# Optimization experiments

Measured on AMD Instinct MI355X. Metric: run time of the kernel, lower is better.

The kernel has to match this reference:

```python
import jax, jax.numpy as jnp
import numpy as np

N_NODES = 100000
N_EDGES = 1600000
N_GRAPHS = 1024
IN_G, HID_G = 64, 128
IN_T, H1, H2 = 200, 256, 128
CONCAT = 2 * HID_G + H2  # 384


def setup_inputs() -> dict:
    key = jax.random.key(0)
    ks = jax.random.split(key, 24)
    def lin(k, fin, fout):
        kw, kb = jax.random.split(k)
        s = 1.0 / np.sqrt(fin)
        return (jax.random.uniform(kw, (fin, fout), jnp.float32, -s, s),
                jax.random.uniform(kb, (fout,), jnp.float32, -s, s))
    Wg1, bg1 = lin(ks[0], IN_G, HID_G)
    Wg2, bg2 = lin(ks[1], HID_G, HID_G)
    Wg3, bg3 = lin(ks[2], HID_G, HID_G)
    Wg4, bg4 = lin(ks[3], HID_G, HID_G)
    Wt1, bt1 = lin(ks[4], IN_T, H1)
    Wt2, bt2 = lin(ks[5], H1, H2)
    Wf1, bf1 = lin(ks[6], CONCAT, H1)
    Wf2, bf2 = lin(ks[7], H1, H2)
    Wf3, bf3 = lin(ks[8], H2, 1)
    x_graph = jax.random.normal(ks[9], (N_NODES, IN_G), jnp.float32)
    edge_index = jax.random.randint(ks[10], (2, N_EDGES), 0, N_NODES, jnp.int32)
    batch = jnp.sort(jax.random.randint(ks[11], (N_NODES,), 0, N_GRAPHS, jnp.int32))
    x_tabular = jax.random.normal(ks[12], (N_GRAPHS, IN_T), jnp.float32)
    return {"x_graph": x_graph, "edge_index": edge_index, "batch": batch,
            "x_tabular": x_tabular,
            "Wg1": Wg1, "bg1": bg1, "Wg2": Wg2, "bg2": bg2,
            "Wg3": Wg3, "bg3": bg3, "Wg4": Wg4, "bg4": bg4,
            "Wt1": Wt1, "bt1": bt1, "Wt2": Wt2, "bt2": bt2,
            "Wf1": Wf1, "bf1": bf1, "Wf2": Wf2, "bf2": bf2,
            "Wf3": Wf3, "bf3": bf3}


def _gcn(x, src, dst, norm, W, b, n):
    # x' = D^-1/2 A_hat D^-1/2 (x W) + b, scatter-add over edges
    h = x @ W
    msg = h[src] * norm[:, None]
    return jax.ops.segment_sum(msg, dst, num_segments=n) + b


def reference(x_graph, edge_index, batch, x_tabular,
              Wg1, bg1, Wg2, bg2, Wg3, bg3, Wg4, bg4,
              Wt1, bt1, Wt2, bt2, Wf1, bf1, Wf2, bf2, Wf3, bf3):
    n = x_graph.shape[0]
    b = x_tabular.shape[0]
    ar = jnp.arange(n, dtype=edge_index.dtype)
    # self-loops added once in Multi_Modal.forward + once inside GCNConv (default)
    src = jnp.concatenate([edge_index[0], ar, ar])
    dst = jnp.concatenate([edge_index[1], ar, ar])
    deg = jax.ops.segment_sum(jnp.ones(src.shape, x_graph.dtype), dst, num_segments=n)
    dinv = jnp.where(deg > 0, jax.lax.rsqrt(deg), 0.0)
    norm = dinv[src] * dinv[dst]
    h = jax.nn.relu(_gcn(x_graph, src, dst, norm, Wg1, bg1, n))
    h = jax.nn.relu(_gcn(h, src, dst, norm, Wg2, bg2, n))
    h = jax.nn.relu(_gcn(h, src, dst, norm, Wg3, bg3, n))
    h = jax.nn.relu(_gcn(h, src, dst, norm, Wg4, bg4, n))
    # global mean/max pool per graph
    cnt = jax.ops.segment_sum(jnp.ones((n,), h.dtype), batch, num_segments=b)
    mean = jax.ops.segment_sum(h, batch, num_segments=b) / jnp.maximum(cnt, 1.0)[:, None]
    mx = jax.ops.segment_max(h, batch, num_segments=b)
    x1 = jnp.concatenate([mean, mx], axis=1)
    # tabular branch
    x2 = jax.nn.relu(jax.nn.relu(x_tabular @ Wt1 + bt1) @ Wt2 + bt2)
    # fused head
    x = jnp.concatenate([x1, x2], axis=1)
    x = jax.nn.relu(x @ Wf1 + bf1)
    x = jax.nn.relu(x @ Wf2 + bf2)
    return jax.nn.sigmoid(x @ Wf3 + bf3)
```

## Files before the change

### kernel.cpp

```cpp
#include <hip/hip_runtime.h>
#include <hip/hip_bf16.h>
#include <math.h>

#define N_NODES  100000
#define N_EDGES  1600000
#define N_GRAPHS 1024

typedef __hip_bfloat16 bf16;
typedef unsigned short u16;
typedef unsigned int   u32;
typedef __attribute__((ext_vector_type(8))) short bf8_t;
typedef __attribute__((ext_vector_type(4))) float f4_t;

__device__ __forceinline__ float b2f(bf16 v) { return __bfloat162float(v); }
__device__ __forceinline__ u16 bfbits(float f) {
    bf16 h = __float2bfloat16(f);
    return *reinterpret_cast<u16*>(&h);
}
__device__ __forceinline__ float lo_bf(u32 u) { return __uint_as_float(u << 16); }
__device__ __forceinline__ float hi_bf(u32 u) { return __uint_as_float(u & 0xffff0000u); }

__global__ void sniff_dtype(const u16* __restrict__ p, int* __restrict__ flag) {
    if (blockIdx.x == 0 && threadIdx.x == 0) {
        int bad = 0;
        for (int i = 0; i < 256; ++i) {
            float f = __uint_as_float(((u32)p[i]) << 16);
            if (!(fabsf(f) < 100.f)) bad++;
        }
        *flag = (bad == 0) ? 1 : 0;
    }
}

#define NT 18
struct WTask { const void* src; void* dst; int n; int mode; int K; };
struct PrepArgs { WTask t[NT]; int bstart[NT]; };

__global__ void prep_k(PrepArgs args, const int* __restrict__ flag) {
    int b = blockIdx.x, ti = 0;
    while (ti < NT - 1 && b >= args.bstart[ti + 1]) ++ti;
    int idx = (b - args.bstart[ti]) * 256 + threadIdx.x;
    WTask tk = args.t[ti];
    if (idx >= tk.n) return;
    int isb = *flag;
    if (tk.mode == 0) {
        float v = isb ? b2f(((const bf16*)tk.src)[idx]) : ((const float*)tk.src)[idx];
        ((float*)tk.dst)[idx] = v;
    } else {
        int bseg = idx >> 9, r = idx & 511;
        int L = r >> 3, j = r & 7;
        int kb = bseg >> 3, tt = bseg & 7;
        int k = kb * 32 + ((L >> 4) << 3) + j;
        int n = (tt << 4) + (L & 15);
        int so = k * 128 + n;
        float v = isb ? b2f(((const bf16*)tk.src)[so]) : ((const float*)tk.src)[so];
        ((u16*)tk.dst)[idx] = bfbits(v);
    }
}

__global__ void cvt_b(const void* __restrict__ src, u16* __restrict__ dst,
                      int n, const int* __restrict__ flag) {
    int i = blockIdx.x * blockDim.x + threadIdx.x;
    if (i >= n) return;
    if (*flag) dst[i] = ((const u16*)src)[i];
    else       dst[i] = bfbits(((const float*)src)[i]);
}

__global__ void deg_init(int* degi) {
    int i = blockIdx.x * blockDim.x + threadIdx.x;
    if (i < N_NODES) degi[i] = 2;
}

__global__ void deg_edges(const int* __restrict__ dst, int* __restrict__ degi) {
    int e = blockIdx.x * blockDim.x + threadIdx.x;
    if (e < N_EDGES) atomicAdd(&degi[dst[e]], 1);
}

__global__ void dinv_k(const int* __restrict__ degi, float* __restrict__ dinv) {
    int i = blockIdx.x * blockDim.x + threadIdx.x;
    if (i < N_NODES) dinv[i] = rsqrtf((float)degi[i]);
}

#define SCAN_B 256
__global__ void scan1(const int* __restrict__ degi, int* __restrict__ ex,
                      int* __restrict__ bsum) {
    __shared__ int s[SCAN_B];
    int i = blockIdx.x * SCAN_B + threadIdx.x;
    int v = (i < N_NODES) ? (degi[i] - 2) : 0;
    s[threadIdx.x] = v;
    __syncthreads();
    for (int off = 1; off < SCAN_B; off <<= 1) {
        int t = (threadIdx.x >= off) ? s[threadIdx.x - off] : 0;
        __syncthreads();
        if (threadIdx.x >= off) s[threadIdx.x] += t;
        __syncthreads();
    }
    if (i < N_NODES) ex[i] = s[threadIdx.x] - v;
    if (threadIdx.x == SCAN_B - 1) bsum[blockIdx.x] = s[SCAN_B - 1];
}

__global__ void scan2(int* __restrict__ bsum, int nb) {
    __shared__ int s[512];
    int i = threadIdx.x;
    int v = (i < nb) ? bsum[i] : 0;
    s[i] = v;
    __syncthreads();
    for (int off = 1; off < 512; off <<= 1) {
        int t = (i >= off) ? s[i - off] : 0;
        __syncthreads();
        if (i >= off) s[i] += t;
        __syncthreads();
    }
    if (i < nb) bsum[i] = s[i] - v;
}

__global__ void scan3(int* __restrict__ rowptr, const int* __restrict__ bsum,
                      int* __restrict__ cnt) {
    int i = blockIdx.x * SCAN_B + threadIdx.x;
    if (i >= N_NODES) return;
    rowptr[i] += bsum[blockIdx.x];
    cnt[i] = 0;
}

__global__ void fill_csr(const int* __restrict__ src, const int* __restrict__ dst,
                         const float* __restrict__ dinv, const int* __restrict__ rowptr,
                         int* __restrict__ cnt, int2* __restrict__ csrp) {
    int e = blockIdx.x * 256 + threadIdx.x;
    if (e >= N_EDGES) return;
    int s = src[e], d = dst[e];
    int pos = rowptr[d] + atomicAdd(&cnt[d], 1);
    csrp[pos] = make_int2(s, __float_as_int(dinv[s] * dinv[d]));
}

template<int K, bool EPI>
__global__ __launch_bounds__(256) void gemm_mfma(const u16* __restrict__ A,
        const u16* __restrict__ Wm, const float* __restrict__ bias,
        u16* __restrict__ Out, int M)
{
    int wave = threadIdx.x >> 6, lane = threadIdx.x & 63;
    int rowBase = blockIdx.x * 64 + wave * 16;
    int quad = lane >> 4, low = lane & 15;
    int arow = rowBase + low;
    if (arow >= M) arow = M - 1;
    const u16* ap = A + (size_t)arow * K + quad * 8;

    f4_t acc[8];
#pragma unroll
    for (int t = 0; t < 8; ++t) acc[t] = (f4_t)(0.f);

#pragma unroll
    for (int kb = 0; kb < K / 32; ++kb) {
        bf8_t a = *(const bf8_t*)(ap + kb * 32);
#pragma unroll
        for (int t = 0; t < 8; ++t) {
            bf8_t b = *(const bf8_t*)(Wm + (((kb << 3) + t) << 9) + lane * 8);
            acc[t] = __builtin_amdgcn_mfma_f32_16x16x32_bf16(a, b, acc[t], 0, 0, 0);
        }
    }

    int orow0 = rowBase + quad * 4;
#pragma unroll
    for (int t = 0; t < 8; ++t) {
        float bn = EPI ? bias[t * 16 + low] : 0.f;
#pragma unroll
        for (int j = 0; j < 4; ++j) {
            int r = orow0 + j;
            float v = acc[t][j];
            if (EPI) v = fmaxf(v + bn, 0.f);
            if (r < M) Out[(size_t)r * 128 + t * 16 + low] = bfbits(v);
        }
    }
}

__global__ __launch_bounds__(256) void gather_x(
        const int* __restrict__ rowptr, const int* __restrict__ cnt,
        const int2* __restrict__ csrp, const u16* __restrict__ X,
        const float* __restrict__ dinv, u16* __restrict__ G)
{
    int node = blockIdx.x * 4 + (threadIdx.x >> 6);
    if (node >= N_NODES) return;
    int lane = threadIdx.x & 63;
    int half = lane >> 5, fi = lane & 31;
    const u32* X2 = (const u32*)X;
    float accx = 0.f, accy = 0.f;
    if (half == 0) {
        float dv = dinv[node];
        float s = 2.f * dv * dv;
        u32 h0 = X2[(size_t)node * 32 + fi];
        accx = s * lo_bf(h0); accy = s * hi_bf(h0);
    }
    int rp = rowptr[node];
    int end = rp + cnt[node];
    int p = rp + half;
    for (; p + 8 <= end; p += 8) {
        int2 m0 = csrp[p],     m1 = csrp[p + 2];
        int2 m2 = csrp[p + 4], m3 = csrp[p + 6];
        u32 v0 = X2[(size_t)m0.x * 32 + fi];
        u32 v1 = X2[(size_t)m1.x * 32 + fi];
        u32 v2 = X2[(size_t)m2.x * 32 + fi];
        u32 v3 = X2[(size_t)m3.x * 32 + fi];
        float w0 = __int_as_float(m0.y), w1 = __int_as_float(m1.y);
        float w2 = __int_as_float(m2.y), w3 = __int_as_float(m3.y);
        accx += w0 * lo_bf(v0) + w1 * lo_bf(v1) + w2 * lo_bf(v2) + w3 * lo_bf(v3);
        accy += w0 * hi_bf(v0) + w1 * hi_bf(v1) + w2 * hi_bf(v2) + w3 * hi_bf(v3);
    }
    for (; p < end; p += 2) {
        int2 m = csrp[p];
        u32 v = X2[(size_t)m.x * 32 + fi];
        float w = __int_as_float(m.y);
        accx += w * lo_bf(v); accy += w * hi_bf(v);
    }
    accx += __shfl_xor(accx, 32);
    accy += __shfl_xor(accy, 32);
    if (half == 0) {
        u32 pack = ((u32)bfbits(accy) << 16) | (u32)bfbits(accx);
        ((u32*)G)[(size_t)node * 32 + fi] = pack;
    }
}

__global__ __launch_bounds__(256) void gather_agg(
        const int* __restrict__ rowptr, const int* __restrict__ cnt,
        const int2* __restrict__ csrp, const u16* __restrict__ H,
        const float* __restrict__ dinv, const float* __restrict__ bias,
        u16* __restrict__ A)
{
    int node = blockIdx.x * 4 + (threadIdx.x >> 6);
    if (node >= N_NODES) return;
    int lane = threadIdx.x & 63;
    const u32* H2 = (const u32*)H;
    float2 bb = ((const float2*)bias)[lane];
    float dv = dinv[node];
    float selfw = 2.f * dv * dv;
    u32 h0 = H2[(size_t)node * 64 + lane];
    float accx = bb.x + selfw * lo_bf(h0);
    float accy = bb.y + selfw * hi_bf(h0);
    int p = rowptr[node];
    int end = p + cnt[node];
    for (; p + 8 <= end; p += 8) {
        int2 m0 = csrp[p],     m1 = csrp[p + 1];
        int2 m2 = csrp[p + 2], m3 = csrp[p + 3];
        int2 m4 = csrp[p + 4], m5 = csrp[p + 5];
        int2 m6 = csrp[p + 6], m7 = csrp[p + 7];
        u32 v0 = H2[(size_t)m0.x * 64 + lane];
        u32 v1 = H2[(size_t)m1.x * 64 + lane];
        u32 v2 = H2[(size_t)m2.x * 64 + lane];
        u32 v3 = H2[(size_t)m3.x * 64 + lane];
        u32 v4 = H2[(size_t)m4.x * 64 + lane];
        u32 v5 = H2[(size_t)m5.x * 64 + lane];
        u32 v6 = H2[(size_t)m6.x * 64 + lane];
        u32 v7 = H2[(size_t)m7.x * 64 + lane];
        float w0 = __int_as_float(m0.y), w1 = __int_as_float(m1.y);
        float w2 = __int_as_float(m2.y), w3 = __int_as_float(m3.y);
        float w4 = __int_as_float(m4.y), w5 = __int_as_float(m5.y);
        float w6 = __int_as_float(m6.y), w7 = __int_as_float(m7.y);
        accx += w0 * lo_bf(v0) + w1 * lo_bf(v1) + w2 * lo_bf(v2) + w3 * lo_bf(v3)
              + w4 * lo_bf(v4) + w5 * lo_bf(v5) + w6 * lo_bf(v6) + w7 * lo_bf(v7);
        accy += w0 * hi_bf(v0) + w1 * hi_bf(v1) + w2 * hi_bf(v2) + w3 * hi_bf(v3)
              + w4 * hi_bf(v4) + w5 * hi_bf(v5) + w6 * hi_bf(v6) + w7 * hi_bf(v7);
    }
    for (; p < end; ++p) {
        int2 m = csrp[p];
        u32 v = H2[(size_t)m.x * 64 + lane];
        float w = __int_as_float(m.y);
        accx += w * lo_bf(v); accy += w * hi_bf(v);
    }
    accx = fmaxf(accx, 0.f);
    accy = fmaxf(accy, 0.f);
    u32 pack = ((u32)bfbits(accy) << 16) | (u32)bfbits(accx);
    ((u32*)A)[(size_t)node * 64 + lane] = pack;
}

__global__ __launch_bounds__(128) void pool_k(const u16* __restrict__ A,
        const int* __restrict__ batch, float* __restrict__ concat)
{
    __shared__ int sb[2];
    int g = blockIdx.x;
    if (threadIdx.x == 0) {
        int lo = 0, hi = N_NODES;
        while (lo < hi) { int m = (lo + hi) >> 1; if (batch[m] < g) lo = m + 1; else hi = m; }
        sb[0] = lo;
        hi = N_NODES;
        while (lo < hi) { int m = (lo + hi) >> 1; if (batch[m] < g + 1) lo = m + 1; else hi = m; }
        sb[1] = lo;
    }
    __syncthreads();
    int start = sb[0], end = sb[1];
    int t = threadIdx.x;
    float sum = 0.f, mx = -3.4e38f;
    for (int n = start; n < end; ++n) {
        float v = __uint_as_float(((u32)A[(size_t)n * 128 + t]) << 16);
        sum += v; mx = fmaxf(mx, v);
    }
    int cnt = end - start;
    float mean = sum / (float)(cnt > 0 ? cnt : 1);
    if (cnt == 0) mx = 0.f;
    concat[g * 384 + t] = mean;
    concat[g * 384 + 128 + t] = mx;
}

template<int KD, bool EXT>
__global__ void rowmm(const void* __restrict__ Xv, int ldx,
                      const float* __restrict__ W, const float* __restrict__ bias,
                      float* __restrict__ out, int ldo, const int* __restrict__ flagp)
{
    extern __shared__ float xs[];
    int g = blockIdx.x;
    int col = threadIdx.x;
    int N = blockDim.x;
    const int isb = EXT ? *flagp : 0;
    for (int k = col; k < KD; k += N) {
        size_t off = (size_t)g * ldx + k;
        xs[k] = EXT ? (isb ? b2f(((const bf16*)Xv)[off]) : ((const float*)Xv)[off])
                    : ((const float*)Xv)[off];
    }
    __syncthreads();
    float acc = bias[col];
    for (int k = 0; k < KD; ++k)
        acc += xs[k] * W[(size_t)k * N + col];
    out[(size_t)g * ldo + col] = fmaxf(acc, 0.f);
}

__global__ __launch_bounds__(256) void head3(const float* __restrict__ u2,
        const float* __restrict__ Wf3, const float* __restrict__ bf3,
        void* __restrict__ out, const int* __restrict__ flagp)
{
    int g = blockIdx.x * 4 + (threadIdx.x >> 6);
    int lane = threadIdx.x & 63;
    float2 v = ((const float2*)(u2 + (size_t)g * 128))[lane];
    float2 w = ((const float2*)Wf3)[lane];
    float acc = v.x * w.x + v.y * w.y;
    for (int off = 32; off > 0; off >>= 1) acc += __shfl_down(acc, off);
    if (lane == 0) {
        float z = acc + bf3[0];
        float sg = 1.f / (1.f + expf(-z));
        if (*flagp) ((bf16*)out)[g] = __float2bfloat16(sg);
        else        ((float*)out)[g] = sg;
    }
}

extern "C" void kernel_launch(void* const* d_in, const int* in_sizes, int n_in,
                              void* d_out, int out_size, void* d_ws, size_t ws_size,
                              hipStream_t stream) {
    const void* x_graph    = d_in[0];
    const int*  edge_index = (const int*)d_in[1];
    const int*  batch      = (const int*)d_in[2];
    const void* x_tab      = d_in[3];

    const int* src  = edge_index;
    const int* dstp = edge_index + N_EDGES;

    char* wsp = (char*)d_ws;
    int*  flag = (int*)wsp;                      wsp += 16;
    u16*  A16  = (u16*)wsp;                      wsp += (size_t)N_NODES * 128 * 2;
    u16*  B16  = (u16*)wsp;                      wsp += (size_t)N_NODES * 128 * 2;
    u16*  X16  = (u16*)wsp;                      wsp += (size_t)N_NODES * 64 * 2;
    u16*  G16  = (u16*)wsp;                      wsp += (size_t)N_NODES * 64 * 2;
    u16*  Wm[4];
    Wm[0] = (u16*)wsp;                           wsp += 64 * 128 * 2;
    Wm[1] = (u16*)wsp;                           wsp += 128 * 128 * 2;
    Wm[2] = (u16*)wsp;                           wsp += 128 * 128 * 2;
    Wm[3] = (u16*)wsp;                           wsp += 128 * 128 * 2;
    float* p = (float*)wsp;
    float* bg1f = p; p += 128;
    float* bg2f = p; p += 128;
    float* bg3f = p; p += 128;
    float* bg4f = p; p += 128;
    float* Wt1f = p; p += 200 * 256; float* bt1f = p; p += 256;
    float* Wt2f = p; p += 256 * 128; float* bt2f = p; p += 128;
    float* Wf1f = p; p += 384 * 256; float* bf1f = p; p += 256;
    float* Wf2f = p; p += 256 * 128; float* bf2f = p; p += 128;
    float* Wf3f = p; p += 128;       float* bf3f = p; p += 4;
    int*   degi   = (int*)p;            p += N_NODES;
    float* dinv   = p;                  p += N_NODES;
    int*   rowptr = (int*)p;            p += N_NODES;
    int*   cnt    = (int*)p;            p += N_NODES;
    int*   bsum   = (int*)p;            p += 512;
    int2*  csrp   = (int2*)p;           p += 2 * N_EDGES;
    float* concat = p;                  p += N_GRAPHS * 384;
    float* t1     = p;                  p += N_GRAPHS * 256;
    float* u1     = p;                  p += N_GRAPHS * 256;
    float* u2     = p;                  p += N_GRAPHS * 128;

    sniff_dtype<<<1, 64, 0, stream>>>((const u16*)x_graph, flag);

    PrepArgs pa;
    auto setT = [&](int i, const void* s, void* d, int n, int mode, int K) {
        pa.t[i].src = s; pa.t[i].dst = d; pa.t[i].n = n; pa.t[i].mode = mode; pa.t[i].K = K;
    };
    setT(0,  d_in[4],  Wm[0], 64 * 128, 1, 64);
    setT(1,  d_in[6],  Wm[1], 128 * 128, 1, 128);
    setT(2,  d_in[8],  Wm[2], 128 * 128, 1, 128);
    setT(3,  d_in[10], Wm[3], 128 * 128, 1, 128);
    setT(4,  d_in[12], Wt1f, 200 * 256, 0, 0);
    setT(5,  d_in[14], Wt2f, 256 * 128, 0, 0);
    setT(6,  d_in[16], Wf1f, 384 * 256, 0, 0);
    setT(7,  d_in[18], Wf2f, 256 * 128, 0, 0);
    setT(8,  d_in[20], Wf3f, 128, 0, 0);
    setT(9,  d_in[5],  bg1f, 128, 0, 0);
    setT(10, d_in[7],  bg2f, 128, 0, 0);
    setT(11, d_in[9],  bg3f, 128, 0, 0);
    setT(12, d_in[11], bg4f, 128, 0, 0);
    setT(13, d_in[13], bt1f, 256, 0, 0);
    setT(14, d_in[15], bt2f, 128, 0, 0);
    setT(15, d_in[17], bf1f, 256, 0, 0);
    setT(16, d_in[19], bf2f, 128, 0, 0);
    setT(17, d_in[21], bf3f, 1, 0, 0);
    int totalBlocks = 0;
    for (int i = 0; i < NT; ++i) {
        pa.bstart[i] = totalBlocks;
        totalBlocks += (pa.t[i].n + 255) / 256;
    }
    prep_k<<<totalBlocks, 256, 0, stream>>>(pa, flag);
    cvt_b<<<(N_NODES * 64 + 255) / 256, 256, 0, stream>>>(x_graph, X16, N_NODES * 64, flag);

    const int nb = (N_NODES + SCAN_B - 1) / SCAN_B;
    deg_init<<<(N_NODES + 255) / 256, 256, 0, stream>>>(degi);
    deg_edges<<<(N_EDGES + 255) / 256, 256, 0, stream>>>(dstp, degi);
    dinv_k<<<(N_NODES + 255) / 256, 256, 0, stream>>>(degi, dinv);
    scan1<<<nb, SCAN_B, 0, stream>>>(degi, rowptr, bsum);
    scan2<<<1, 512, 0, stream>>>(bsum, nb);
    scan3<<<nb, SCAN_B, 0, stream>>>(rowptr, bsum, cnt);
    fill_csr<<<(N_EDGES + 255) / 256, 256, 0, stream>>>(src, dstp, dinv, rowptr, cnt, csrp);

    const int gemmGrid = (N_NODES + 63) / 64;
    const int aggGrid  = (N_NODES + 3) / 4;

    gather_x<<<aggGrid, 256, 0, stream>>>(rowptr, cnt, csrp, X16, dinv, G16);
    gemm_mfma<64, true><<<gemmGrid, 256, 0, stream>>>(G16, Wm[0], bg1f, A16, N_NODES);

    const float* bgL[4] = {bg1f, bg2f, bg3f, bg4f};
    for (int l = 1; l < 4; ++l) {
        gemm_mfma<128, false><<<gemmGrid, 256, 0, stream>>>(A16, Wm[l], nullptr, B16, N_NODES);
        gather_agg<<<aggGrid, 256, 0, stream>>>(rowptr, cnt, csrp, B16, dinv, bgL[l], A16);
    }

    pool_k<<<N_GRAPHS, 128, 0, stream>>>(A16, batch, concat);

    rowmm<200, true><<<N_GRAPHS, 256, 200 * 4, stream>>>(x_tab, 200, Wt1f, bt1f, t1, 256, flag);
    rowmm<256, false><<<N_GRAPHS, 128, 256 * 4, stream>>>(t1, 256, Wt2f, bt2f, concat + 256, 384, flag);

    rowmm<384, false><<<N_GRAPHS, 256, 384 * 4, stream>>>(concat, 384, Wf1f, bf1f, u1, 256, flag);
    rowmm<256, false><<<N_GRAPHS, 128, 256 * 4, stream>>>(u1, 256, Wf2f, bf2f, u2, 128, flag);
    head3<<<N_GRAPHS / 4, 256, 0, stream>>>(u2, Wf3f, bf3f, d_out, flag);
}
```

Baseline: 772.7 us.

## Pack CSR entries into 32-bit words and fuse setup and tail kernels

Each CSR entry now packs the source index (17 bits) with a 15-bit quantised dinv[src] into one u32, and dinv[dst] is applied once per node after the gather. This halves edge-stream bytes in every aggregation pass at the cost of quantising the normalisation weight. Several small launches are also merged: degree init goes into the sniff kernel, dinv into scan1, and the x conversion into prep_k. Pooling, the tabular MLP and the fused head now run in one per-graph tail kernel, and pooling uses two halves of the block.

Result: faster. 733.4 us (-5.1%).

```diff
diff --git a/kernel.cpp b/kernel.cpp
--- a/kernel.cpp
+++ b/kernel.cpp
@@ -20,19 +20,22 @@
 __device__ __forceinline__ float lo_bf(u32 u) { return __uint_as_float(u << 16); }
 __device__ __forceinline__ float hi_bf(u32 u) { return __uint_as_float(u & 0xffff0000u); }
 
-__global__ void sniff_dtype(const u16* __restrict__ p, int* __restrict__ flag) {
+__global__ void sniff_init(const u16* __restrict__ xg, int* __restrict__ flag,
+                           int* __restrict__ degi) {
+    int i = blockIdx.x * 256 + threadIdx.x;
+    if (i < N_NODES) degi[i] = 2;
     if (blockIdx.x == 0 && threadIdx.x == 0) {
         int bad = 0;
-        for (int i = 0; i < 256; ++i) {
-            float f = __uint_as_float(((u32)p[i]) << 16);
+        for (int k = 0; k < 256; ++k) {
+            float f = __uint_as_float(((u32)xg[k]) << 16);
             if (!(fabsf(f) < 100.f)) bad++;
         }
         *flag = (bad == 0) ? 1 : 0;
     }
 }
 
-#define NT 18
-struct WTask { const void* src; void* dst; int n; int mode; int K; };
+#define NT 19
+struct WTask { const void* src; void* dst; int n; int mode; };
 struct PrepArgs { WTask t[NT]; int bstart[NT]; };
 
 __global__ void prep_k(PrepArgs args, const int* __restrict__ flag) {
@@ -45,7 +48,7 @@
     if (tk.mode == 0) {
         float v = isb ? b2f(((const bf16*)tk.src)[idx]) : ((const float*)tk.src)[idx];
         ((float*)tk.dst)[idx] = v;
-    } else {
+    } else if (tk.mode == 1) {
         int bseg = idx >> 9, r = idx & 511;
         int L = r >> 3, j = r & 7;
         int kb = bseg >> 3, tt = bseg & 7;
@@ -54,20 +57,10 @@
         int so = k * 128 + n;
         float v = isb ? b2f(((const bf16*)tk.src)[so]) : ((const float*)tk.src)[so];
         ((u16*)tk.dst)[idx] = bfbits(v);
-    }
-}
-
-__global__ void cvt_b(const void* __restrict__ src, u16* __restrict__ dst,
-                      int n, const int* __restrict__ flag) {
-    int i = blockIdx.x * blockDim.x + threadIdx.x;
-    if (i >= n) return;
-    if (*flag) dst[i] = ((const u16*)src)[i];
-    else       dst[i] = bfbits(((const float*)src)[i]);
-}
-
-__global__ void deg_init(int* degi) {
-    int i = blockIdx.x * blockDim.x + threadIdx.x;
-    if (i < N_NODES) degi[i] = 2;
+    } else {
+        u16 v = isb ? ((const u16*)tk.src)[idx] : bfbits(((const float*)tk.src)[idx]);
+        ((u16*)tk.dst)[idx] = v;
+    }
 }
 
 __global__ void deg_edges(const int* __restrict__ dst, int* __restrict__ degi) {
@@ -75,17 +68,13 @@
     if (e < N_EDGES) atomicAdd(&degi[dst[e]], 1);
 }
 
-__global__ void dinv_k(const int* __restrict__ degi, float* __restrict__ dinv) {
-    int i = blockIdx.x * blockDim.x + threadIdx.x;
-    if (i < N_NODES) dinv[i] = rsqrtf((float)degi[i]);
-}
-
 #define SCAN_B 256
 __global__ void scan1(const int* __restrict__ degi, int* __restrict__ ex,
-                      int* __restrict__ bsum) {
+                      int* __restrict__ bsum, float* __restrict__ dinv) {
     __shared__ int s[SCAN_B];
     int i = blockIdx.x * SCAN_B + threadIdx.x;
-    int v = (i < N_NODES) ? (degi[i] - 2) : 0;
+    int dg = (i < N_NODES) ? degi[i] : 2;
+    int v = dg - 2;
     s[threadIdx.x] = v;
     __syncthreads();
     for (int off = 1; off < SCAN_B; off <<= 1) {
@@ -94,7 +83,10 @@
         if (threadIdx.x >= off) s[threadIdx.x] += t;
         __syncthreads();
     }
-    if (i < N_NODES) ex[i] = s[threadIdx.x] - v;
+    if (i < N_NODES) {
+        ex[i] = s[threadIdx.x] - v;
+        dinv[i] = rsqrtf((float)dg);
+    }
     if (threadIdx.x == SCAN_B - 1) bsum[blockIdx.x] = s[SCAN_B - 1];
 }
 
@@ -123,12 +115,13 @@
 
 __global__ void fill_csr(const int* __restrict__ src, const int* __restrict__ dst,
                          const float* __restrict__ dinv, const int* __restrict__ rowptr,
-                         int* __restrict__ cnt, int2* __restrict__ csrp) {
+                         int* __restrict__ cnt, u32* __restrict__ csr4) {
     int e = blockIdx.x * 256 + threadIdx.x;
     if (e >= N_EDGES) return;
     int s = src[e], d = dst[e];
     int pos = rowptr[d] + atomicAdd(&cnt[d], 1);
-    csrp[pos] = make_int2(s, __float_as_int(dinv[s] * dinv[d]));
+    u32 q = (u32)__float2int_rn(dinv[s] * 32767.f);
+    csr4[pos] = (q << 17) | (u32)s;
 }
 
 template<int K, bool EPI>
@@ -171,55 +164,9 @@
     }
 }
 
-__global__ __launch_bounds__(256) void gather_x(
-        const int* __restrict__ rowptr, const int* __restrict__ cnt,
-        const int2* __restrict__ csrp, const u16* __restrict__ X,
-        const float* __restrict__ dinv, u16* __restrict__ G)
-{
-    int node = blockIdx.x * 4 + (threadIdx.x >> 6);
-    if (node >= N_NODES) return;
-    int lane = threadIdx.x & 63;
-    int half = lane >> 5, fi = lane & 31;
-    const u32* X2 = (const u32*)X;
-    float accx = 0.f, accy = 0.f;
-    if (half == 0) {
-        float dv = dinv[node];
-        float s = 2.f * dv * dv;
-        u32 h0 = X2[(size_t)node * 32 + fi];
-        accx = s * lo_bf(h0); accy = s * hi_bf(h0);
-    }
-    int rp = rowptr[node];
-    int end = rp + cnt[node];
-    int p = rp + half;
-    for (; p + 8 <= end; p += 8) {
-        int2 m0 = csrp[p],     m1 = csrp[p + 2];
-        int2 m2 = csrp[p + 4], m3 = csrp[p + 6];
-        u32 v0 = X2[(size_t)m0.x * 32 + fi];
-        u32 v1 = X2[(size_t)m1.x * 32 + fi];
-        u32 v2 = X2[(size_t)m2.x * 32 + fi];
-        u32 v3 = X2[(size_t)m3.x * 32 + fi];
-        float w0 = __int_as_float(m0.y), w1 = __int_as_float(m1.y);
-        float w2 = __int_as_float(m2.y), w3 = __int_as_float(m3.y);
-        accx += w0 * lo_bf(v0) + w1 * lo_bf(v1) + w2 * lo_bf(v2) + w3 * lo_bf(v3);
-        accy += w0 * hi_bf(v0) + w1 * hi_bf(v1) + w2 * hi_bf(v2) + w3 * hi_bf(v3);
-    }
-    for (; p < end; p += 2) {
-        int2 m = csrp[p];
-        u32 v = X2[(size_t)m.x * 32 + fi];
-        float w = __int_as_float(m.y);
-        accx += w * lo_bf(v); accy += w * hi_bf(v);
-    }
-    accx += __shfl_xor(accx, 32);
-    accy += __shfl_xor(accy, 32);
-    if (half == 0) {
-        u32 pack = ((u32)bfbits(accy) << 16) | (u32)bfbits(accx);
-        ((u32*)G)[(size_t)node * 32 + fi] = pack;
-    }
-}
-
 __global__ __launch_bounds__(256) void gather_agg(
         const int* __restrict__ rowptr, const int* __restrict__ cnt,
-        const int2* __restrict__ csrp, const u16* __restrict__ H,
+        const u32* __restrict__ csr4, const u16* __restrict__ H,
         const float* __restrict__ dinv, const float* __restrict__ bias,
         u16* __restrict__ A)
 {
@@ -229,52 +176,112 @@
     const u32* H2 = (const u32*)H;
     float2 bb = ((const float2*)bias)[lane];
     float dv = dinv[node];
-    float selfw = 2.f * dv * dv;
     u32 h0 = H2[(size_t)node * 64 + lane];
-    float accx = bb.x + selfw * lo_bf(h0);
-    float accy = bb.y + selfw * hi_bf(h0);
+    float accx = 2.f * dv * lo_bf(h0);
+    float accy = 2.f * dv * hi_bf(h0);
     int p = rowptr[node];
     int end = p + cnt[node];
+    const float qs = 1.f / 32767.f;
     for (; p + 8 <= end; p += 8) {
-        int2 m0 = csrp[p],     m1 = csrp[p + 1];
-        int2 m2 = csrp[p + 2], m3 = csrp[p + 3];
-        int2 m4 = csrp[p + 4], m5 = csrp[p + 5];
-        int2 m6 = csrp[p + 6], m7 = csrp[p + 7];
-        u32 v0 = H2[(size_t)m0.x * 64 + lane];
-        u32 v1 = H2[(size_t)m1.x * 64 + lane];
-        u32 v2 = H2[(size_t)m2.x * 64 + lane];
-        u32 v3 = H2[(size_t)m3.x * 64 + lane];
-        u32 v4 = H2[(size_t)m4.x * 64 + lane];
-        u32 v5 = H2[(size_t)m5.x * 64 + lane];
-        u32 v6 = H2[(size_t)m6.x * 64 + lane];
-        u32 v7 = H2[(size_t)m7.x * 64 + lane];
-        float w0 = __int_as_float(m0.y), w1 = __int_as_float(m1.y);
-        float w2 = __int_as_float(m2.y), w3 = __int_as_float(m3.y);
-        float w4 = __int_as_float(m4.y), w5 = __int_as_float(m5.y);
-        float w6 = __int_as_float(m6.y), w7 = __int_as_float(m7.y);
+        u32 m0 = csr4[p],     m1 = csr4[p + 1];
+        u32 m2 = csr4[p + 2], m3 = csr4[p + 3];
+        u32 m4 = csr4[p + 4], m5 = csr4[p + 5];
+        u32 m6 = csr4[p + 6], m7 = csr4[p + 7];
+        u32 v0 = H2[(size_t)(m0 & 0x1FFFFu) * 64 + lane];
+        u32 v1 = H2[(size_t)(m1 & 0x1FFFFu) * 64 + lane];
+        u32 v2 = H2[(size_t)(m2 & 0x1FFFFu) * 64 + lane];
+        u32 v3 = H2[(size_t)(m3 & 0x1FFFFu) * 64 + lane];
+        u32 v4 = H2[(size_t)(m4 & 0x1FFFFu) * 64 + lane];
+        u32 v5 = H2[(size_t)(m5 & 0x1FFFFu) * 64 + lane];
+        u32 v6 = H2[(size_t)(m6 & 0x1FFFFu) * 64 + lane];
+        u32 v7 = H2[(size_t)(m7 & 0x1FFFFu) * 64 + lane];
+        float w0 = (float)(m0 >> 17) * qs, w1 = (float)(m1 >> 17) * qs;
+        float w2 = (float)(m2 >> 17) * qs, w3 = (float)(m3 >> 17) * qs;
+        float w4 = (float)(m4 >> 17) * qs, w5 = (float)(m5 >> 17) * qs;
+        float w6 = (float)(m6 >> 17) * qs, w7 = (float)(m7 >> 17) * qs;
         accx += w0 * lo_bf(v0) + w1 * lo_bf(v1) + w2 * lo_bf(v2) + w3 * lo_bf(v3)
               + w4 * lo_bf(v4) + w5 * lo_bf(v5) + w6 * lo_bf(v6) + w7 * lo_bf(v7);
         accy += w0 * hi_bf(v0) + w1 * hi_bf(v1) + w2 * hi_bf(v2) + w3 * hi_bf(v3)
               + w4 * hi_bf(v4) + w5 * hi_bf(v5) + w6 * hi_bf(v6) + w7 * hi_bf(v7);
     }
     for (; p < end; ++p) {
-        int2 m = csrp[p];
-        u32 v = H2[(size_t)m.x * 64 + lane];
-        float w = __int_as_float(m.y);
+        u32 m = csr4[p];
+        u32 v = H2[(size_t)(m & 0x1FFFFu) * 64 + lane];
+        float w = (float)(m >> 17) * qs;
         accx += w * lo_bf(v); accy += w * hi_bf(v);
     }
-    accx = fmaxf(accx, 0.f);
-    accy = fmaxf(accy, 0.f);
+    accx = fmaxf(accx * dv + bb.x, 0.f);
+    accy = fmaxf(accy * dv + bb.y, 0.f);
     u32 pack = ((u32)bfbits(accy) << 16) | (u32)bfbits(accx);
     ((u32*)A)[(size_t)node * 64 + lane] = pack;
 }
 
-__global__ __launch_bounds__(128) void pool_k(const u16* __restrict__ A,
-        const int* __restrict__ batch, float* __restrict__ concat)
+__global__ __launch_bounds__(256) void gather_x(
+        const int* __restrict__ rowptr, const int* __restrict__ cnt,
+        const u32* __restrict__ csr4, const u16* __restrict__ X,
+        const float* __restrict__ dinv, u16* __restrict__ G)
 {
+    int node = blockIdx.x * 4 + (threadIdx.x >> 6);
+    if (node >= N_NODES) return;
+    int lane = threadIdx.x & 63;
+    int half = lane >> 5, fi = lane & 31;
+    const u32* X2 = (const u32*)X;
+    float dv = dinv[node];
+    float accx = 0.f, accy = 0.f;
+    if (half == 0) {
+        u32 h0 = X2[(size_t)node * 32 + fi];
+        accx = 2.f * dv * lo_bf(h0); accy = 2.f * dv * hi_bf(h0);
+    }
+    int rp = rowptr[node];
+    int end = rp + cnt[node];
+    const float qs = 1.f / 32767.f;
+    int p = rp + half;
+    for (; p + 6 < end; p += 8) {
+        u32 m0 = csr4[p],     m1 = csr4[p + 2];
+        u32 m2 = csr4[p + 4], m3 = csr4[p + 6];
+        u32 v0 = X2[(size_t)(m0 & 0x1FFFFu) * 32 + fi];
+        u32 v1 = X2[(size_t)(m1 & 0x1FFFFu) * 32 + fi];
+        u32 v2 = X2[(size_t)(m2 & 0x1FFFFu) * 32 + fi];
+        u32 v3 = X2[(size_t)(m3 & 0x1FFFFu) * 32 + fi];
+        float w0 = (float)(m0 >> 17) * qs, w1 = (float)(m1 >> 17) * qs;
+        float w2 = (float)(m2 >> 17) * qs, w3 = (float)(m3 >> 17) * qs;
+        accx += w0 * lo_bf(v0) + w1 * lo_bf(v1) + w2 * lo_bf(v2) + w3 * lo_bf(v3);
+        accy += w0 * hi_bf(v0) + w1 * hi_bf(v1) + w2 * hi_bf(v2) + w3 * hi_bf(v3);
+    }
+    for (; p < end; p += 2) {
+        u32 m = csr4[p];
+        u32 v = X2[(size_t)(m & 0x1FFFFu) * 32 + fi];
+        float w = (float)(m >> 17) * qs;
+        accx += w * lo_bf(v); accy += w * hi_bf(v);
+    }
+    accx += __shfl_xor(accx, 32);
+    accy += __shfl_xor(accy, 32);
+    if (half == 0) {
+        accx *= dv; accy *= dv;
+        u32 pack = ((u32)bfbits(accy) << 16) | (u32)bfbits(accx);
+        ((u32*)G)[(size_t)node * 32 + fi] = pack;
+    }
+}
+
+__global__ __launch_bounds__(256) void tail_k(const u16* __restrict__ A,
+        const int* __restrict__ batch, const void* __restrict__ x_tab,
+        const float* __restrict__ Wt1, const float* __restrict__ bt1,
+        const float* __restrict__ Wt2, const float* __restrict__ bt2,
+        const float* __restrict__ Wf1, const float* __restrict__ bf1,
+        const float* __restrict__ Wf2, const float* __restrict__ bf2,
+        const float* __restrict__ Wf3, const float* __restrict__ bf3,
+        void* __restrict__ out, const int* __restrict__ flagp)
+{
+    __shared__ float xs[384];
+    __shared__ float t1s[256];
+    __shared__ float u1s[256];
+    __shared__ float u2s[128];
+    __shared__ float xts[200];
+    __shared__ float ps[256], pm[256];
     __shared__ int sb[2];
     int g = blockIdx.x;
-    if (threadIdx.x == 0) {
+    int tid = threadIdx.x;
+    if (tid == 0) {
         int lo = 0, hi = N_NODES;
         while (lo < hi) { int m = (lo + hi) >> 1; if (batch[m] < g) lo = m + 1; else hi = m; }
         sb[0] = lo;
@@ -282,58 +289,56 @@
         while (lo < hi) { int m = (lo + hi) >> 1; if (batch[m] < g + 1) lo = m + 1; else hi = m; }
         sb[1] = lo;
     }
+    int isb = *flagp;
+    if (tid < 200)
+        xts[tid] = isb ? b2f(((const bf16*)x_tab)[(size_t)g * 200 + tid])
+                       : ((const float*)x_tab)[(size_t)g * 200 + tid];
     __syncthreads();
     int start = sb[0], end = sb[1];
-    int t = threadIdx.x;
+    int t = tid & 127, half = tid >> 7;
     float sum = 0.f, mx = -3.4e38f;
-    for (int n = start; n < end; ++n) {
+    for (int n = start + half; n < end; n += 2) {
         float v = __uint_as_float(((u32)A[(size_t)n * 128 + t]) << 16);
         sum += v; mx = fmaxf(mx, v);
     }
-    int cnt = end - start;
-    float mean = sum / (float)(cnt > 0 ? cnt : 1);
-    if (cnt == 0) mx = 0.f;
-    concat[g * 384 + t] = mean;
-    concat[g * 384 + 128 + t] = mx;
-}
-
-template<int KD, bool EXT>
-__global__ void rowmm(const void* __restrict__ Xv, int ldx,
-                      const float* __restrict__ W, const float* __restrict__ bias,
-                      float* __restrict__ out, int ldo, const int* __restrict__ flagp)
-{
-    extern __shared__ float xs[];
-    int g = blockIdx.x;
-    int col = threadIdx.x;
-    int N = blockDim.x;
-    const int isb = EXT ? *flagp : 0;
-    for (int k = col; k < KD; k += N) {
-        size_t off = (size_t)g * ldx + k;
-        xs[k] = EXT ? (isb ? b2f(((const bf16*)Xv)[off]) : ((const float*)Xv)[off])
-                    : ((const float*)Xv)[off];
-    }
-    __syncthreads();
-    float acc = bias[col];
-    for (int k = 0; k < KD; ++k)
-        acc += xs[k] * W[(size_t)k * N + col];
-    out[(size_t)g * ldo + col] = fmaxf(acc, 0.f);
-}
-
-__global__ __launch_bounds__(256) void head3(const float* __restrict__ u2,
-        const float* __restrict__ Wf3, const float* __restrict__ bf3,
-        void* __restrict__ out, const int* __restrict__ flagp)
-{
-    int g = blockIdx.x * 4 + (threadIdx.x >> 6);
-    int lane = threadIdx.x & 63;
-    float2 v = ((const float2*)(u2 + (size_t)g * 128))[lane];
-    float2 w = ((const float2*)Wf3)[lane];
-    float acc = v.x * w.x + v.y * w.y;
-    for (int off = 32; off > 0; off >>= 1) acc += __shfl_down(acc, off);
-    if (lane == 0) {
-        float z = acc + bf3[0];
-        float sg = 1.f / (1.f + expf(-z));
-        if (*flagp) ((bf16*)out)[g] = __float2bfloat16(sg);
-        else        ((float*)out)[g] = sg;
+    ps[tid] = sum; pm[tid] = mx;
+    __syncthreads();
+    if (half == 0) {
+        int c = end - start;
+        float s2 = ps[t] + ps[t + 128];
+        float m2 = fmaxf(pm[t], pm[t + 128]);
+        xs[t] = s2 / (float)(c > 0 ? c : 1);
+        xs[128 + t] = (c > 0) ? m2 : 0.f;
+    }
+    float acc = bt1[tid];
+    for (int k = 0; k < 200; ++k) acc += xts[k] * Wt1[k * 256 + tid];
+    t1s[tid] = fmaxf(acc, 0.f);
+    __syncthreads();
+    if (tid < 128) {
+        acc = bt2[tid];
+        for (int k = 0; k < 256; ++k) acc += t1s[k] * Wt2[k * 128 + tid];
+        xs[256 + tid] = fmaxf(acc, 0.f);
+    }
+    __syncthreads();
+    acc = bf1[tid];
+    for (int k = 0; k < 384; ++k) acc += xs[k] * Wf1[k * 256 + tid];
+    u1s[tid] = fmaxf(acc, 0.f);
+    __syncthreads();
+    if (tid < 128) {
+        acc = bf2[tid];
+        for (int k = 0; k < 256; ++k) acc += u1s[k] * Wf2[k * 128 + tid];
+        u2s[tid] = fmaxf(acc, 0.f);
+    }
+    __syncthreads();
+    if (tid < 64) {
+        float a = u2s[tid] * Wf3[tid] + u2s[tid + 64] * Wf3[tid + 64];
+        for (int off = 32; off > 0; off >>= 1) a += __shfl_down(a, off);
+        if (tid == 0) {
+            float z = a + bf3[0];
+            float sg = 1.f / (1.f + expf(-z));
+            if (isb) ((bf16*)out)[g] = __float2bfloat16(sg);
+            else     ((float*)out)[g] = sg;
+        }
     }
 }
 
@@ -374,71 +379,59 @@
     int*   rowptr = (int*)p;            p += N_NODES;
     int*   cnt    = (int*)p;            p += N_NODES;
     int*   bsum   = (int*)p;            p += 512;
-    int2*  csrp   = (int2*)p;           p += 2 * N_EDGES;
-    float* concat = p;                  p += N_GRAPHS * 384;
-    float* t1     = p;                  p += N_GRAPHS * 256;
-    float* u1     = p;                  p += N_GRAPHS * 256;
-    float* u2     = p;                  p += N_GRAPHS * 128;
-
-    sniff_dtype<<<1, 64, 0, stream>>>((const u16*)x_graph, flag);
+    u32*   csr4   = (u32*)p;            p += N_EDGES;
+
+    sniff_init<<<(N_NODES + 255) / 256, 256, 0, stream>>>((const u16*)x_graph, flag, degi);
 
     PrepArgs pa;
-    auto setT = [&](int i, const void* s, void* d, int n, int mode, int K) {
-        pa.t[i].src = s; pa.t[i].dst = d; pa.t[i].n = n; pa.t[i].mode = mode; pa.t[i].K = K;
+    auto setT = [&](int i, const void* s, void* d, int n, int mode) {
+        pa.t[i].src = s; pa.t[i].dst = d; pa.t[i].n = n; pa.t[i].mode = mode;
     };
-    setT(0,  d_in[4],  Wm[0], 64 * 128, 1, 64);
-    setT(1,  d_in[6],  Wm[1], 128 * 128, 1, 128);
-    setT(2,  d_in[8],  Wm[2], 128 * 128, 1, 128);
-    setT(3,  d_in[10], Wm[3], 128 * 128, 1, 128);
-    setT(4,  d_in[12], Wt1f, 200 * 256, 0, 0);
-    setT(5,  d_in[14], Wt2f, 256 * 128, 0, 0);
-    setT(6,  d_in[16], Wf1f, 384 * 256, 0, 0);
-    setT(7,  d_in[18], Wf2f, 256 * 128, 0, 0);
-    setT(8,  d_in[20], Wf3f, 128, 0, 0);
-    setT(9,  d_in[5],  bg1f, 128, 0, 0);
-    setT(10, d_in[7],  bg2f, 128, 0, 0);
-    setT(11, d_in[9],  bg3f, 128, 0, 0);
-    setT(12, d_in[11], bg4f, 128, 0, 0);
-    setT(13, d_in[13], bt1f, 256, 0, 0);
-    setT(14, d_in[15], bt2f, 128, 0, 0);
-    setT(15, d_in[17], bf1f, 256, 0, 0);
-    setT(16, d_in[19], bf2f, 128, 0, 0);
-    setT(17, d_in[21], bf3f, 1, 0, 0);
+    setT(0,  d_in[4],  Wm[0], 64 * 128, 1);
+    setT(1,  d_in[6],  Wm[1], 128 * 128, 1);
+    setT(2,  d_in[8],  Wm[2], 128 * 128, 1);
+    setT(3,  d_in[10], Wm[3], 128 * 128, 1);
+    setT(4,  d_in[12], Wt1f, 200 * 256, 0);
+    setT(5,  d_in[14], Wt2f, 256 * 128, 0);
+    setT(6,  d_in[16], Wf1f, 384 * 256, 0);
+    setT(7,  d_in[18], Wf2f, 256 * 128, 0);
+    setT(8,  d_in[20], Wf3f, 128, 0);
+    setT(9,  d_in[5],  bg1f, 128, 0);
+    setT(10, d_in[7],  bg2f, 128, 0);
+    setT(11, d_in[9],  bg3f, 128, 0);
+    setT(12, d_in[11], bg4f, 128, 0);
+    setT(13, d_in[13], bt1f, 256, 0);
+    setT(14, d_in[15], bt2f, 128, 0);
+    setT(15, d_in[17], bf1f, 256, 0);
+    setT(16, d_in[19], bf2f, 128, 0);
+    setT(17, d_in[21], bf3f, 1, 0);
+    setT(18, d_in[0],  X16, N_NODES * 64, 2);
     int totalBlocks = 0;
     for (int i = 0; i < NT; ++i) {
         pa.bstart[i] = totalBlocks;
         totalBlocks += (pa.t[i].n + 255) / 256;
     }
     prep_k<<<totalBlocks, 256, 0, stream>>>(pa, flag);
-    cvt_b<<<(N_NODES * 64 + 255) / 256, 256, 0, stream>>>(x_graph, X16, N_NODES * 64, flag);
 
     const int nb = (N_NODES + SCAN_B - 1) / SCAN_B;
-    deg_init<<<(N_NODES + 255) / 256, 256, 0, stream>>>(degi);
     deg_edges<<<(N_EDGES + 255) / 256, 256, 0, stream>>>(dstp, degi);
-    dinv_k<<<(N_NODES + 255) / 256, 256, 0, stream>>>(degi, dinv);
-    scan1<<<nb, SCAN_B, 0, stream>>>(degi, rowptr, bsum);
+    scan1<<<nb, SCAN_B, 0, stream>>>(degi, rowptr, bsum, dinv);
     scan2<<<1, 512, 0, stream>>>(bsum, nb);
     scan3<<<nb, SCAN_B, 0, stream>>>(rowptr, bsum, cnt);
-    fill_csr<<<(N_EDGES + 255) / 256, 256, 0, stream>>>(src, dstp, dinv, rowptr, cnt, csrp);
+    fill_csr<<<(N_EDGES + 255) / 256, 256, 0, stream>>>(src, dstp, dinv, rowptr, cnt, csr4);
 
     const int gemmGrid = (N_NODES + 63) / 64;
     const int aggGrid  = (N_NODES + 3) / 4;
 
-    gather_x<<<aggGrid, 256, 0, stream>>>(rowptr, cnt, csrp, X16, dinv, G16);
+    gather_x<<<aggGrid, 256, 0, stream>>>(rowptr, cnt, csr4, X16, dinv, G16);
     gemm_mfma<64, true><<<gemmGrid, 256, 0, stream>>>(G16, Wm[0], bg1f, A16, N_NODES);
 
     const float* bgL[4] = {bg1f, bg2f, bg3f, bg4f};
     for (int l = 1; l < 4; ++l) {
         gemm_mfma<128, false><<<gemmGrid, 256, 0, stream>>>(A16, Wm[l], nullptr, B16, N_NODES);
-        gather_agg<<<aggGrid, 256, 0, stream>>>(rowptr, cnt, csrp, B16, dinv, bgL[l], A16);
-    }
-
-    pool_k<<<N_GRAPHS, 128, 0, stream>>>(A16, batch, concat);
-
-    rowmm<200, true><<<N_GRAPHS, 256, 200 * 4, stream>>>(x_tab, 200, Wt1f, bt1f, t1, 256, flag);
-    rowmm<256, false><<<N_GRAPHS, 128, 256 * 4, stream>>>(t1, 256, Wt2f, bt2f, concat + 256, 384, flag);
-
-    rowmm<384, false><<<N_GRAPHS, 256, 384 * 4, stream>>>(concat, 384, Wf1f, bf1f, u1, 256, flag);
-    rowmm<256, false><<<N_GRAPHS, 128, 256 * 4, stream>>>(u1, 256, Wf2f, bf2f, u2, 128, flag);
-    head3<<<N_GRAPHS / 4, 256, 0, stream>>>(u2, Wf3f, bf3f, d_out, flag);
-}
+        gather_agg<<<aggGrid, 256, 0, stream>>>(rowptr, cnt, csr4, B16, dinv, bgL[l], A16);
+    }
+
+    tail_k<<<N_GRAPHS, 256, 0, stream>>>(A16, batch, x_tab,
+        Wt1f, bt1f, Wt2f, bt2f, Wf1f, bf1f, Wf2f, bf2f, Wf3f, bf3f, d_out, flag);
+}
```
